# Performance work log

Measured on AMD Instinct MI355X. Metric: run time of the kernel, lower is better.

## Reference

```python
import jax, jax.numpy as jnp
import numpy as np

B, N, C, H = 2, 2048, 1024, 16
D = C // H  # head_dim = 64


def setup_inputs() -> dict:
    key = jax.random.key(0)
    kx, kq, kk, kv, ko = jax.random.split(key, 5)
    # xavier_uniform bound for square (C, C) matrices
    bound = float(np.sqrt(6.0 / (C + C)))
    u = lambda k: jax.random.uniform(k, (C, C), jnp.float32, -bound, bound)
    return {
        "x": jax.random.normal(kx, (B, N, C), jnp.float32),
        "W_q": u(kq),
        "W_k": u(kk),
        "W_v": u(kv),
        "W_o": u(ko),
    }


def reference(x, W_q, W_k, W_v, W_o):
    # quantum_linear == dense matmul (no bias); tomography_error_delta=0 -> identity
    b, n, c = x.shape
    q = jnp.einsum("bnc,cd->bnd", x, W_q).reshape(b, n, H, D).transpose(0, 2, 1, 3)
    k = jnp.einsum("bnc,cd->bnd", x, W_k).reshape(b, n, H, D).transpose(0, 2, 1, 3)
    v = jnp.einsum("bnc,cd->bnd", x, W_v).reshape(b, n, H, D).transpose(0, 2, 1, 3)
    # scaled dot-product attention, [B, H, N, N]
    scores = jnp.einsum("bhnd,bhmd->bhnm", q, k) / jnp.sqrt(jnp.float32(D))
    weights = jax.nn.softmax(scores, axis=-1)
    heads = jnp.einsum("bhnm,bhmd->bhnd", weights, v)  # [B, H, N, D]
    concat = heads.transpose(0, 2, 1, 3).reshape(b, n, c)
    out = jnp.einsum("bnc,cd->bnd", concat, W_o)
    return out
```

## Files before the change

### kernel.cpp

```cpp
#include <hip/hip_runtime.h>

typedef __attribute__((ext_vector_type(4))) float f32x4;
typedef __attribute__((ext_vector_type(8))) short s16x8;
typedef unsigned int u32;
typedef __attribute__((ext_vector_type(4))) unsigned int u32x4;

#define B_ 2
#define N_ 2048
#define C_ 1024
#define H_ 16
#define D_ 64

__device__ __forceinline__ unsigned short f2bf(float f) {
  union { float f; unsigned u; } v; v.f = f;
  unsigned r = v.u + 0x7fffu + ((v.u >> 16) & 1u);
  return (unsigned short)(r >> 16);
}

__global__ __launch_bounds__(256) void wtrans_kernel(
    const float* __restrict__ Wq, const float* __restrict__ Wk,
    const float* __restrict__ Wv, const float* __restrict__ Wo,
    unsigned short* __restrict__ WtQKV, unsigned short* __restrict__ WtO,
    const float* __restrict__ xsrc, unsigned short* __restrict__ xb) {
  const int t = threadIdx.x;
  if (blockIdx.x >= 1024) {
    int i = (blockIdx.x - 1024) * 2048 + t * 8;
    float4 f0 = *(const float4*)&xsrc[i];
    float4 f1 = *(const float4*)&xsrc[i + 4];
    u32 p0, p1, p2, p3;
    asm("v_cvt_pk_bf16_f32 %0, %1, %2" : "=v"(p0) : "v"(f0.x), "v"(f0.y));
    asm("v_cvt_pk_bf16_f32 %0, %1, %2" : "=v"(p1) : "v"(f0.z), "v"(f0.w));
    asm("v_cvt_pk_bf16_f32 %0, %1, %2" : "=v"(p2) : "v"(f1.x), "v"(f1.y));
    asm("v_cvt_pk_bf16_f32 %0, %1, %2" : "=v"(p3) : "v"(f1.z), "v"(f1.w));
    uint4 o; o.x = p0; o.y = p1; o.z = p2; o.w = p3;
    *(uint4*)&xb[i] = o;
    return;
  }
  __shared__ float lds[64][65];
  const int w = blockIdx.x >> 8;
  const int tile = blockIdx.x & 255;
  const int c0 = (tile >> 4) * 64, d0 = (tile & 15) * 64;
  const float* W = (w == 0) ? Wq : (w == 1) ? Wk : (w == 2) ? Wv : Wo;
  const float scale = (w == 0) ? 0.125f * 1.4426950408889634f : 1.0f;
  #pragma unroll
  for (int p = 0; p < 16; ++p) {
    int i = p * 256 + t; int r = i >> 6, cc = i & 63;
    lds[r][cc] = W[(size_t)(c0 + r) * 1024 + d0 + cc];
  }
  __syncthreads();
  #pragma unroll
  for (int p = 0; p < 16; ++p) {
    int i = p * 256 + t; int r = i >> 6, cc = i & 63;
    unsigned short v = f2bf(lds[cc][r] * scale);
    if (w < 3) WtQKV[(size_t)(w * 1024 + d0 + r) * 1024 + c0 + cc] = v;
    else       WtO[(size_t)(d0 + r) * 1024 + c0 + cc] = v;
  }
}

template <int MODE>
__global__ __launch_bounds__(256, 3) void gemm_kernel(
    const unsigned short* __restrict__ A, const unsigned short* __restrict__ Bt,
    unsigned short* __restrict__ Qh, unsigned short* __restrict__ Kh,
    unsigned short* __restrict__ Vt, float* __restrict__ Cf) {
  __shared__ unsigned short As[2][128 * 32];
  __shared__ unsigned short Bs[2][128 * 32];
  const int tid = threadIdx.x;
  const int lane = tid & 63, wv = tid >> 6;
  const int g = lane >> 4, c = lane & 15;
  const int wr = wv >> 1, wc = wv & 1;
  const int am0 = blockIdx.x * 128;
  const int bn0 = blockIdx.y * 128;

  f32x4 acc[4][4];
  #pragma unroll
  for (int m = 0; m < 4; m++)
    #pragma unroll
    for (int n = 0; n < 4; n++) acc[m][n] = (f32x4){0.f, 0.f, 0.f, 0.f};

  const int srow = (lane >> 2);
  const int schunk = (lane & 3) ^ (srow & 3);

#define GSTAGE(buf, k0s)                                                       \
  do {                                                                         \
    _Pragma("unroll")                                                          \
    for (int i = 0; i < 2; ++i) {                                              \
      int row = i * 64 + wv * 16 + srow;                                       \
      __builtin_amdgcn_global_load_lds(                                        \
          (const __attribute__((address_space(1))) void*)(                     \
              A + (size_t)(am0 + row) * 1024 + (k0s) + schunk * 8),            \
          (__attribute__((address_space(3))) void*)(&As[buf][(i * 64 + wv * 16) * 32]), \
          16, 0, 0);                                                           \
      __builtin_amdgcn_global_load_lds(                                        \
          (const __attribute__((address_space(1))) void*)(                     \
              Bt + (size_t)(bn0 + row) * 1024 + (k0s) + schunk * 8),           \
          (__attribute__((address_space(3))) void*)(&Bs[buf][(i * 64 + wv * 16) * 32]), \
          16, 0, 0);                                                           \
    }                                                                          \
  } while (0)

  GSTAGE(0, 0);
  __syncthreads();
  for (int kt = 0; kt < 32; ++kt) {
    const int cur = kt & 1;
    if (kt < 31) GSTAGE(cur ^ 1, (kt + 1) * 32);
    s16x8 af[4], bfr[4];
    #pragma unroll
    for (int m = 0; m < 4; m++) {
      int R = wr * 64 + m * 16 + c;
      af[m] = *(const s16x8*)&As[cur][R * 32 + ((g ^ (R & 3)) << 3)];
    }
    #pragma unroll
    for (int n = 0; n < 4; n++) {
      int R = wc * 64 + n * 16 + c;
      bfr[n] = *(const s16x8*)&Bs[cur][R * 32 + ((g ^ (R & 3)) << 3)];
    }
    __builtin_amdgcn_s_setprio(1);
    #pragma unroll
    for (int m = 0; m < 4; m++)
      #pragma unroll
      for (int n = 0; n < 4; n++)
        acc[m][n] = __builtin_amdgcn_mfma_f32_16x16x32_bf16(af[m], bfr[n], acc[m][n], 0, 0, 0);
    __builtin_amdgcn_s_setprio(0);
    __syncthreads();
  }
#undef GSTAGE

  #pragma unroll
  for (int m = 0; m < 4; m++) {
    #pragma unroll
    for (int n = 0; n < 4; n++) {
      f32x4 v = acc[m][n];
      int colg = bn0 + wc * 64 + n * 16 + c;
      #pragma unroll
      for (int r = 0; r < 4; ++r) {
        int row = am0 + wr * 64 + m * 16 + g * 4 + r;
        if (MODE == 1) {
          Cf[(size_t)row * 1024 + colg] = v[r];
        } else {
          int tensor = colg >> 10, cc = colg & 1023;
          int hh = cc >> 6, dd = cc & 63;
          int bb = row >> 11, tok = row & 2047;
          unsigned short val = f2bf(v[r]);
          if (tensor == 0)
            Qh[(((size_t)bb * H_ + hh) * N_ + tok) * D_ + dd] = val;
          else if (tensor == 1)
            Kh[(((size_t)bb * H_ + hh) * N_ + tok) * D_ + dd] = val;
          else
            Vt[(((size_t)bb * H_ + hh) * D_ + dd) * N_ + tok] = val;
        }
      }
    }
  }
}

__global__ __launch_bounds__(512, 2) void attn_kernel(
    const unsigned short* __restrict__ Qh, const unsigned short* __restrict__ Kh,
    const unsigned short* __restrict__ Vt, unsigned short* __restrict__ heads) {
  __shared__ unsigned short Ks[2][128 * 64];
  __shared__ unsigned short Vs[2][64 * 128];
  const int tid = threadIdx.x;
  const int lane = tid & 63, wv = tid >> 6;
  const int g = lane >> 4, c = lane & 15;
  const int c7 = c & 7;
  const int xcd = blockIdx.x & 7, idx = blockIdx.x >> 3;
  const int bh = xcd * 4 + (idx >> 3), qb = idx & 7;
  const int b = bh >> 4, h = bh & 15;
  const int q0 = qb * 256 + wv * 32;

  const unsigned short* Qbase = Qh + ((size_t)bh * N_ + q0) * D_;
  const unsigned short* Kbase = Kh + (size_t)bh * N_ * D_;
  const unsigned short* Vbase = Vt + (size_t)bh * D_ * N_;

  s16x8 qfrag[2][2];
  #pragma unroll
  for (int qf = 0; qf < 2; ++qf)
    #pragma unroll
    for (int dblk = 0; dblk < 2; ++dblk)
      qfrag[qf][dblk] =
          *(const s16x8*)&Qbase[(size_t)(qf * 16 + c) * D_ + dblk * 32 + g * 8];

  s16x8 ones;
  #pragma unroll
  for (int j = 0; j < 8; ++j) ones[j] = (short)0x3F80;

  f32x4 O[2][4];
  f32x4 L[2];
  #pragma unroll
  for (int qf = 0; qf < 2; ++qf) {
    #pragma unroll
    for (int db = 0; db < 4; ++db) O[qf][db] = (f32x4){0.f, 0.f, 0.f, 0.f};
    L[qf] = (f32x4){0.f, 0.f, 0.f, 0.f};
  }

#define STAGE(buf, t)                                                          \
  do {                                                                         \
    const int kv0s = (t) * 128;                                                \
    _Pragma("unroll")                                                          \
    for (int i = 0; i < 2; ++i) {                                              \
      int row = i * 64 + wv * 8 + (lane >> 3);                                 \
      int un = (lane & 7) ^ (row & 7);                                         \
      __builtin_amdgcn_global_load_lds(                                        \
          (const __attribute__((address_space(1))) void*)(Kbase +              \
              (size_t)(kv0s + row) * 64 + un * 8),                             \
          (__attribute__((address_space(3))) void*)(&Ks[buf][(i * 512 + wv * 64) * 8]), \
          16, 0, 0);                                                           \
    }                                                                          \
    _Pragma("unroll")                                                          \
    for (int i = 0; i < 2; ++i) {                                              \
      int vrow = i * 32 + wv * 4 + (lane >> 4);                                \
      int un = (lane & 15) ^ (vrow & 15);                                      \
      __builtin_amdgcn_global_load_lds(                                        \
          (const __attribute__((address_space(1))) void*)(Vbase +              \
              (size_t)vrow * N_ + kv0s + un * 8),                              \
          (__attribute__((address_space(3))) void*)(&Vs[buf][(i * 512 + wv * 64) * 8]), \
          16, 0, 0);                                                           \
    }                                                                          \
  } while (0)

  STAGE(0, 0);
  __syncthreads();

  for (int t = 0; t < 16; ++t) {
    const int cur = t & 1;
    if (t < 15) STAGE(cur ^ 1, t + 1);

    f32x4 st[2][8];
    __builtin_amdgcn_s_setprio(1);
    #pragma unroll
    for (int kb = 0; kb < 8; ++kb) {
      s16x8 k0 = *(const s16x8*)&Ks[cur][(kb * 16 + c) * 64 + ((g ^ c7) << 3)];
      s16x8 k1 = *(const s16x8*)&Ks[cur][(kb * 16 + c) * 64 + (((4 + g) ^ c7) << 3)];
      #pragma unroll
      for (int qf = 0; qf < 2; ++qf) {
        f32x4 z = (f32x4){0.f, 0.f, 0.f, 0.f};
        z = __builtin_amdgcn_mfma_f32_16x16x32_bf16(k0, qfrag[qf][0], z, 0, 0, 0);
        st[qf][kb] = __builtin_amdgcn_mfma_f32_16x16x32_bf16(k1, qfrag[qf][1], z, 0, 0, 0);
      }
    }
    __builtin_amdgcn_s_setprio(0);

    u32 pf[2][4][4];
    #pragma unroll
    for (int qf = 0; qf < 2; ++qf) {
      #pragma unroll
      for (int kb = 0; kb < 8; ++kb)
        #pragma unroll
        for (int r = 0; r < 4; ++r)
          st[qf][kb][r] = __builtin_amdgcn_exp2f(st[qf][kb][r]);

      #pragma unroll
      for (int km = 0; km < 4; ++km) {
        u32 x00, x01, x10, x11;
        asm("v_cvt_pk_bf16_f32 %0, %1, %2" : "=v"(x00) : "v"(st[qf][2 * km][0]), "v"(st[qf][2 * km][1]));
        asm("v_cvt_pk_bf16_f32 %0, %1, %2" : "=v"(x01) : "v"(st[qf][2 * km][2]), "v"(st[qf][2 * km][3]));
        asm("v_cvt_pk_bf16_f32 %0, %1, %2" : "=v"(x10) : "v"(st[qf][2 * km + 1][0]), "v"(st[qf][2 * km + 1][1]));
        asm("v_cvt_pk_bf16_f32 %0, %1, %2" : "=v"(x11) : "v"(st[qf][2 * km + 1][2]), "v"(st[qf][2 * km + 1][3]));
        asm("v_permlane32_swap_b32 %0, %1" : "+v"(x00), "+v"(x10));
        asm("v_permlane32_swap_b32 %0, %1" : "+v"(x01), "+v"(x11));
        asm("v_permlane16_swap_b32 %0, %1" : "+v"(x00), "+v"(x10));
        asm("v_permlane16_swap_b32 %0, %1" : "+v"(x01), "+v"(x11));
        pf[qf][km][0] = x00; pf[qf][km][1] = x01;
        pf[qf][km][2] = x10; pf[qf][km][3] = x11;
      }
    }

    __builtin_amdgcn_s_setprio(1);
    #pragma unroll
    for (int km = 0; km < 4; ++km) {
      union { u32x4 u; s16x8 s; } b0, b1;
      b0.u = (u32x4){pf[0][km][0], pf[0][km][1], pf[0][km][2], pf[0][km][3]};
      b1.u = (u32x4){pf[1][km][0], pf[1][km][1], pf[1][km][2], pf[1][km][3]};
      #pragma unroll
      for (int db = 0; db < 4; ++db) {
        s16x8 vf = *(const s16x8*)&Vs[cur][(db * 16 + c) * 128 + (((km * 4 + g) ^ c) << 3)];
        O[0][db] = __builtin_amdgcn_mfma_f32_16x16x32_bf16(vf, b0.s, O[0][db], 0, 0, 0);
        O[1][db] = __builtin_amdgcn_mfma_f32_16x16x32_bf16(vf, b1.s, O[1][db], 0, 0, 0);
      }
      L[0] = __builtin_amdgcn_mfma_f32_16x16x32_bf16(ones, b0.s, L[0], 0, 0, 0);
      L[1] = __builtin_amdgcn_mfma_f32_16x16x32_bf16(ones, b1.s, L[1], 0, 0, 0);
    }
    __builtin_amdgcn_s_setprio(0);
    __syncthreads();
  }
#undef STAGE

  #pragma unroll
  for (int qf = 0; qf < 2; ++qf) {
    float linv = 1.0f / L[qf][0];
    size_t rowoff = ((size_t)(b * N_ + q0 + qf * 16 + c)) * C_ + h * 64;
    #pragma unroll
    for (int db = 0; db < 4; ++db) {
      u32 d0, d1;
      float v0 = O[qf][db][0] * linv, v1 = O[qf][db][1] * linv;
      float v2 = O[qf][db][2] * linv, v3 = O[qf][db][3] * linv;
      asm("v_cvt_pk_bf16_f32 %0, %1, %2" : "=v"(d0) : "v"(v0), "v"(v1));
      asm("v_cvt_pk_bf16_f32 %0, %1, %2" : "=v"(d1) : "v"(v2), "v"(v3));
      uint2 st2; st2.x = d0; st2.y = d1;
      *(uint2*)&heads[rowoff + db * 16 + g * 4] = st2;
    }
  }
}

extern "C" void kernel_launch(void* const* d_in, const int* in_sizes, int n_in,
                              void* d_out, int out_size, void* d_ws, size_t ws_size,
                              hipStream_t stream) {
  const float* x  = (const float*)d_in[0];
  const float* Wq = (const float*)d_in[1];
  const float* Wk = (const float*)d_in[2];
  const float* Wv = (const float*)d_in[3];
  const float* Wo = (const float*)d_in[4];
  float* out = (float*)d_out;

  char* ws = (char*)d_ws;
  unsigned short* WtQKV = (unsigned short*)(ws);
  unsigned short* WtO   = (unsigned short*)(ws + 6291456);
  unsigned short* Qh    = (unsigned short*)(ws + 8388608);
  unsigned short* Kh    = (unsigned short*)(ws + 16777216);
  unsigned short* Vt    = (unsigned short*)(ws + 25165824);
  unsigned short* heads = (unsigned short*)(ws + 33554432);
  unsigned short* xb    = (unsigned short*)(ws + 33554432);

  wtrans_kernel<<<dim3(3072), dim3(256), 0, stream>>>(Wq, Wk, Wv, Wo, WtQKV, WtO, x, xb);
  gemm_kernel<0><<<dim3(32, 24), dim3(256), 0, stream>>>(xb, WtQKV, Qh, Kh, Vt, nullptr);
  attn_kernel<<<dim3(256), dim3(512), 0, stream>>>(Qh, Kh, Vt, heads);
  gemm_kernel<1><<<dim3(32, 8), dim3(256), 0, stream>>>(heads, WtO, nullptr, nullptr, nullptr, out);
}
```

Measured before the change: 115.0 us.

## Software-pipeline attention so PV of the previous tile overlaps the current softmax

Restructures the attention loop so that the P·V MFMAs for tile t-1 are issued after tile t's QK^T MFMAs and before tile t's exp and bf16 packing. The goal is to interleave matrix-core work with the VALU exponentials and permlane shuffles instead of running them back to back. V is triple-buffered in LDS, so the tile-(t-1) V buffer stays valid while tile t+1 is being prefetched, and the last PV step is drained after the loop. The loop is fully unrolled and keeps an extra copy of the packed probabilities. This raises LDS use to about 80KB per block and adds register pressure under the 512x2 launch bounds, which could cause spills or lower occupancy.

```diff
diff --git a/kernel.cpp b/kernel.cpp
--- a/kernel.cpp
+++ b/kernel.cpp
@@ -157,7 +157,7 @@
     const unsigned short* __restrict__ Qh, const unsigned short* __restrict__ Kh,
     const unsigned short* __restrict__ Vt, unsigned short* __restrict__ heads) {
   __shared__ unsigned short Ks[2][128 * 64];
-  __shared__ unsigned short Vs[2][64 * 128];
+  __shared__ unsigned short Vs[3][64 * 128];
   const int tid = threadIdx.x;
   const int lane = tid & 63, wv = tid >> 6;
   const int g = lane >> 4, c = lane & 15;
@@ -192,7 +192,7 @@
     L[qf] = (f32x4){0.f, 0.f, 0.f, 0.f};
   }
 
-#define STAGE(buf, t)                                                          \
+#define STAGE(kbuf, vbuf, t)                                                   \
   do {                                                                         \
     const int kv0s = (t) * 128;                                                \
     _Pragma("unroll")                                                          \
@@ -202,7 +202,7 @@
       __builtin_amdgcn_global_load_lds(                                        \
           (const __attribute__((address_space(1))) void*)(Kbase +              \
               (size_t)(kv0s + row) * 64 + un * 8),                             \
-          (__attribute__((address_space(3))) void*)(&Ks[buf][(i * 512 + wv * 64) * 8]), \
+          (__attribute__((address_space(3))) void*)(&Ks[kbuf][(i * 512 + wv * 64) * 8]), \
           16, 0, 0);                                                           \
     }                                                                          \
     _Pragma("unroll")                                                          \
@@ -212,24 +212,46 @@
       __builtin_amdgcn_global_load_lds(                                        \
           (const __attribute__((address_space(1))) void*)(Vbase +              \
               (size_t)vrow * N_ + kv0s + un * 8),                              \
-          (__attribute__((address_space(3))) void*)(&Vs[buf][(i * 512 + wv * 64) * 8]), \
+          (__attribute__((address_space(3))) void*)(&Vs[vbuf][(i * 512 + wv * 64) * 8]), \
           16, 0, 0);                                                           \
     }                                                                          \
   } while (0)
 
-  STAGE(0, 0);
+#define PVSTEP(VBUF, PF)                                                       \
+  do {                                                                         \
+    _Pragma("unroll")                                                          \
+    for (int km = 0; km < 4; ++km) {                                           \
+      union { u32x4 u; s16x8 s; } b0_, b1_;                                    \
+      b0_.u = (u32x4){PF[0][km][0], PF[0][km][1], PF[0][km][2], PF[0][km][3]}; \
+      b1_.u = (u32x4){PF[1][km][0], PF[1][km][1], PF[1][km][2], PF[1][km][3]}; \
+      _Pragma("unroll")                                                        \
+      for (int db = 0; db < 4; ++db) {                                         \
+        s16x8 vf = *(const s16x8*)&Vs[VBUF][(db * 16 + c) * 128 +              \
+                                           (((km * 4 + g) ^ c) << 3)];         \
+        O[0][db] = __builtin_amdgcn_mfma_f32_16x16x32_bf16(vf, b0_.s, O[0][db], 0, 0, 0); \
+        O[1][db] = __builtin_amdgcn_mfma_f32_16x16x32_bf16(vf, b1_.s, O[1][db], 0, 0, 0); \
+      }                                                                        \
+      L[0] = __builtin_amdgcn_mfma_f32_16x16x32_bf16(ones, b0_.s, L[0], 0, 0, 0); \
+      L[1] = __builtin_amdgcn_mfma_f32_16x16x32_bf16(ones, b1_.s, L[1], 0, 0, 0); \
+    }                                                                          \
+  } while (0)
+
+  u32 pf[2][4][4], pfp[2][4][4];
+
+  STAGE(0, 0, 0);
   __syncthreads();
 
+  #pragma unroll
   for (int t = 0; t < 16; ++t) {
-    const int cur = t & 1;
-    if (t < 15) STAGE(cur ^ 1, t + 1);
+    const int kcur = t & 1;
+    if (t < 15) STAGE((t + 1) & 1, (t + 1) % 3, t + 1);
 
     f32x4 st[2][8];
     __builtin_amdgcn_s_setprio(1);
     #pragma unroll
     for (int kb = 0; kb < 8; ++kb) {
-      s16x8 k0 = *(const s16x8*)&Ks[cur][(kb * 16 + c) * 64 + ((g ^ c7) << 3)];
-      s16x8 k1 = *(const s16x8*)&Ks[cur][(kb * 16 + c) * 64 + (((4 + g) ^ c7) << 3)];
+      s16x8 k0 = *(const s16x8*)&Ks[kcur][(kb * 16 + c) * 64 + ((g ^ c7) << 3)];
+      s16x8 k1 = *(const s16x8*)&Ks[kcur][(kb * 16 + c) * 64 + (((4 + g) ^ c7) << 3)];
       #pragma unroll
       for (int qf = 0; qf < 2; ++qf) {
         f32x4 z = (f32x4){0.f, 0.f, 0.f, 0.f};
@@ -239,7 +261,10 @@
     }
     __builtin_amdgcn_s_setprio(0);
 
-    u32 pf[2][4][4];
+    if (t > 0) {
+      PVSTEP((t + 2) % 3, pfp);
+    }
+
     #pragma unroll
     for (int qf = 0; qf < 2; ++qf) {
       #pragma unroll
@@ -264,25 +289,21 @@
       }
     }
 
-    __builtin_amdgcn_s_setprio(1);
-    #pragma unroll
-    for (int km = 0; km < 4; ++km) {
-      union { u32x4 u; s16x8 s; } b0, b1;
-      b0.u = (u32x4){pf[0][km][0], pf[0][km][1], pf[0][km][2], pf[0][km][3]};
-      b1.u = (u32x4){pf[1][km][0], pf[1][km][1], pf[1][km][2], pf[1][km][3]};
-      #pragma unroll
-      for (int db = 0; db < 4; ++db) {
-        s16x8 vf = *(const s16x8*)&Vs[cur][(db * 16 + c) * 128 + (((km * 4 + g) ^ c) << 3)];
-        O[0][db] = __builtin_amdgcn_mfma_f32_16x16x32_bf16(vf, b0.s, O[0][db], 0, 0, 0);
-        O[1][db] = __builtin_amdgcn_mfma_f32_16x16x32_bf16(vf, b1.s, O[1][db], 0, 0, 0);
-      }
-      L[0] = __builtin_amdgcn_mfma_f32_16x16x32_bf16(ones, b0.s, L[0], 0, 0, 0);
-      L[1] = __builtin_amdgcn_mfma_f32_16x16x32_bf16(ones, b1.s, L[1], 0, 0, 0);
-    }
-    __builtin_amdgcn_s_setprio(0);
+    #pragma unroll
+    for (int qf = 0; qf < 2; ++qf)
+      #pragma unroll
+      for (int km = 0; km < 4; ++km)
+        #pragma unroll
+        for (int j = 0; j < 4; ++j) pfp[qf][km][j] = pf[qf][km][j];
+
     __syncthreads();
   }
+
+  __builtin_amdgcn_s_setprio(1);
+  PVSTEP(0, pfp);
+  __builtin_amdgcn_s_setprio(0);
 #undef STAGE
+#undef PVSTEP
 
   #pragma unroll
   for (int qf = 0; qf < 2; ++qf) {
```

Measured after the change: 109.5 us. -4.8%, faster.
